# Optimization experiments

Hardware: AMD Instinct MI355X
Metric: run time of the kernel (lower is better)

## Reference

```python
import jax, jax.numpy as jnp
import numpy as np

THRESHOLD = 0.5
NEG_POS_RATIO = 3
ALPHA = 1.0
BETA = 1.0
IGNORE_INDEX = 255

B, P, C, O = 16, 16384, 21, 16
H = W = 256


def cxcy_to_xy(c):
    return jnp.concatenate([c[..., :2] - c[..., 2:] / 2, c[..., :2] + c[..., 2:] / 2], axis=-1)


def xy_to_cxcy(xy):
    return jnp.concatenate([(xy[..., :2] + xy[..., 2:]) / 2, xy[..., 2:] - xy[..., :2]], axis=-1)


def cxcy_to_gcxgcy(cxcy, priors_cxcy):
    return jnp.concatenate([
        (cxcy[..., :2] - priors_cxcy[..., :2]) / (priors_cxcy[..., 2:] / 10.0),
        jnp.log(cxcy[..., 2:] / priors_cxcy[..., 2:]) * 5.0,
    ], axis=-1)


def jaccard(set1, set2):
    # set1 [O,4] xy, set2 [P,4] xy -> IoU [O,P]
    lo = jnp.maximum(set1[:, None, :2], set2[None, :, :2])
    hi = jnp.minimum(set1[:, None, 2:], set2[None, :, 2:])
    wh = jnp.clip(hi - lo, 0.0)
    inter = wh[..., 0] * wh[..., 1]
    a1 = (set1[:, 2] - set1[:, 0]) * (set1[:, 3] - set1[:, 1])
    a2 = (set2[:, 2] - set2[:, 0]) * (set2[:, 3] - set2[:, 1])
    return inter / (a1[:, None] + a2[None, :] - inter)


def setup_inputs() -> dict:
    key = jax.random.key(0)
    ks = jax.random.split(key, 8)
    predicted_locs = jax.random.normal(ks[0], (B, P, 4), dtype=jnp.float32)
    predicted_scores = jax.random.normal(ks[1], (B, P, C), dtype=jnp.float32)
    predicted_masks = jax.random.normal(ks[2], (B, C, H, W), dtype=jnp.float32)
    x1y1 = jax.random.uniform(ks[3], (B, O, 2), dtype=jnp.float32) * 0.8
    wh = jax.random.uniform(ks[4], (B, O, 2), dtype=jnp.float32) * 0.19 + 0.01
    boxes = jnp.concatenate([x1y1, x1y1 + wh], axis=-1)  # valid xy boxes
    pc = jax.random.uniform(ks[5], (P, 2), dtype=jnp.float32) * 0.9 + 0.05
    pwh = jax.random.uniform(ks[6], (P, 2), dtype=jnp.float32) * 0.28 + 0.02
    priors_cxcy = jnp.concatenate([pc, pwh], axis=-1)
    labels = jax.random.randint(ks[7], (B, O), 1, C)  # object labels, never background
    masks = jax.random.randint(jax.random.fold_in(key, 99), (B, 1, H, W), 0, C)
    return {
        'predicted_locs': predicted_locs,
        'predicted_scores': predicted_scores,
        'predicted_masks': predicted_masks,
        'boxes': boxes,
        'priors_cxcy': priors_cxcy,
        'labels': labels,
        'masks': masks,
    }


def _assign(bx, lb, priors_cxcy, priors_xy):
    # bx [O,4] xy, lb [O] int -> true_locs [P,4], true_classes [P]
    ov = jaccard(bx, priors_xy)  # [O,P]
    overlap_for_each_prior = ov.max(axis=0)       # [P]
    object_for_each_prior = ov.argmax(axis=0)     # [P]
    prior_for_each_object = ov.argmax(axis=1)     # [O]
    # guarantee every object is matched to its best prior
    object_for_each_prior = object_for_each_prior.at[prior_for_each_object].set(jnp.arange(O))
    overlap_for_each_prior = overlap_for_each_prior.at[prior_for_each_object].set(1.0)
    label_for_each_prior = lb[object_for_each_prior]
    label_for_each_prior = jnp.where(overlap_for_each_prior < THRESHOLD, 0, label_for_each_prior)
    true_locs = cxcy_to_gcxgcy(xy_to_cxcy(bx[object_for_each_prior]), priors_cxcy)
    return true_locs, label_for_each_prior


def reference(predicted_locs, predicted_scores, predicted_masks, boxes, priors_cxcy, labels, masks):
    priors_xy = cxcy_to_xy(priors_cxcy)
    true_locs, true_classes = jax.vmap(_assign, in_axes=(0, 0, None, None))(
        boxes, labels, priors_cxcy, priors_xy)  # [B,P,4], [B,P]

    pos = true_classes != 0                      # [B,P]
    pos_f = pos.astype(predicted_locs.dtype)
    n_pos = pos.sum(axis=1)                      # [B]

    # localization: L1Loss (mean over positive prior elements)
    diff = jnp.abs(predicted_locs - true_locs)
    loc_loss = (diff * pos_f[..., None]).sum() / jnp.maximum(pos_f.sum() * 4.0, 1.0)

    # confidence: CE per prior + hard negative mining
    logp = jax.nn.log_softmax(predicted_scores, axis=-1)            # [B,P,C]
    ce = -jnp.take_along_axis(logp, true_classes[..., None], axis=-1)[..., 0]  # [B,P]
    ce_pos_sum = (ce * pos_f).sum()
    ce_neg = jnp.where(pos, 0.0, ce)
    ce_neg_sorted = -jnp.sort(-ce_neg, axis=1)                      # descending
    ranks = jnp.arange(P)[None, :]
    hard = (ranks < (NEG_POS_RATIO * n_pos)[:, None]).astype(ce.dtype)
    ce_hardneg_sum = (ce_neg_sorted * hard).sum()
    conf_loss = (ce_hardneg_sum + ce_pos_sum) / n_pos.sum().astype(ce.dtype)

    # mask loss: cross_entropy2d, sum reduction then / (H*W) / B
    tgt = masks[:, 0]                                                # [B,H,W]
    valid = (tgt != IGNORE_INDEX)
    t = jnp.where(valid, tgt, 0)
    logp_m = jax.nn.log_softmax(predicted_masks, axis=1)             # [B,C,H,W]
    ce_m = -jnp.take_along_axis(logp_m, t[:, None], axis=1)[:, 0]    # [B,H,W]
    mask_loss = (ce_m * valid.astype(ce_m.dtype)).sum() / (H * W) / B

    return conf_loss + ALPHA * loc_loss + BETA * mask_loss
```

## Files before the change

kernel.cpp:

```cpp
#include <hip/hip_runtime.h>
#include <cstdint>
#include <cstddef>

#define Bn 16
#define Pn 16384
#define Cn 21
#define On 16
#define HWn 65536
#define THRESH 0.5f


__device__ __forceinline__ float waveReduceSum(float v) {
  for (int off = 32; off > 0; off >>= 1) v += __shfl_down(v, off, 64);
  return v;
}
__device__ __forceinline__ int waveReduceSumI(int v) {
  for (int off = 32; off > 0; off >>= 1) v += __shfl_down(v, off, 64);
  return v;
}

__global__ __launch_bounds__(256) void k_phase1(
    const float* __restrict__ boxes, const float* __restrict__ priors,
    unsigned long long* __restrict__ partials, int* __restrict__ done_cnt) {
  const int lane = threadIdx.x & 63, wave = threadIdx.x >> 6;
  __shared__ float4 sbox[On];
  __shared__ float sarea[On];
  __shared__ unsigned long long skey[On];
  if (blockIdx.x == 0 && threadIdx.x == 0) *done_cnt = 0;

  const int b = blockIdx.x >> 6;
  const int p0 = (blockIdx.x & 63) << 8;
  const int p = p0 + threadIdx.x;
  if (threadIdx.x < On) {
    float4 bx = ((const float4*)boxes)[b * On + threadIdx.x];
    sbox[threadIdx.x] = bx;
    sarea[threadIdx.x] = (bx.z - bx.x) * (bx.w - bx.y);
    skey[threadIdx.x] = 0ULL;
  }
  __syncthreads();
  float4 pr = ((const float4*)priors)[p];
  const float px1 = pr.x - 0.5f * pr.z, py1 = pr.y - 0.5f * pr.w;
  const float px2 = pr.x + 0.5f * pr.z, py2 = pr.y + 0.5f * pr.w;
  const float parea = pr.z * pr.w;
#pragma unroll
  for (int o = 0; o < On; ++o) {
    float4 bx = sbox[o];
    float ix = fmaxf(fminf(px2, bx.z) - fmaxf(px1, bx.x), 0.f);
    float iy = fmaxf(fminf(py2, bx.w) - fmaxf(py1, bx.y), 0.f);
    float inter = ix * iy;
    float iou = inter / (sarea[o] + parea - inter);
    float m = iou;
#pragma unroll
    for (int off = 32; off > 0; off >>= 1) m = fmaxf(m, __shfl_xor(m, off, 64));
    unsigned long long tie = __ballot(iou == m);
    if (lane == 0) {
      int lmin = __ffsll(tie) - 1;
      unsigned minp = (unsigned)(p0 + (wave << 6) + lmin);
      unsigned long long key = ((unsigned long long)__float_as_uint(m) << 32) |
                               (unsigned long long)(0xFFFFFFFFu - minp);
      atomicMax(&skey[o], key);
    }
  }
  __syncthreads();
  if (threadIdx.x < On)
    partials[(size_t)blockIdx.x * On + threadIdx.x] = skey[threadIdx.x];
}

__global__ __launch_bounds__(256, 2) void k_assign(
    const float* __restrict__ plocs, const float* __restrict__ pscores,
    const float* __restrict__ boxes, const float* __restrict__ priors,
    const int* __restrict__ labels, const unsigned long long* __restrict__ partials,
    float* __restrict__ ce_neg, float* __restrict__ apart_loc,
    float* __restrict__ apart_ce, int* __restrict__ apart_npos) {
  __shared__ float ssc[256 * Cn];
  __shared__ float4 sbox[On];
  __shared__ float sarea[On];
  __shared__ int slab[On];
  __shared__ int spfo[On];
  __shared__ unsigned long long skey[On];
  __shared__ float sr1[4], sr2[4];
  __shared__ int sri[4];
  const int lane = threadIdx.x & 63, wave = threadIdx.x >> 6;
  const int b = blockIdx.x >> 6;
  const int p0 = (blockIdx.x & 63) << 8;
  const int p = p0 + threadIdx.x;
  {
    const float4* src = (const float4*)(pscores + ((size_t)b * Pn + p0) * Cn);
    float4* dst = (float4*)ssc;
#pragma unroll
    for (int i = threadIdx.x; i < (256 * Cn) / 4; i += 256) dst[i] = src[i];
  }
  if (threadIdx.x < On) {
    float4 bx = ((const float4*)boxes)[b * On + threadIdx.x];
    sbox[threadIdx.x] = bx;
    sarea[threadIdx.x] = (bx.z - bx.x) * (bx.w - bx.y);
    slab[threadIdx.x] = labels[b * On + threadIdx.x];
    skey[threadIdx.x] = 0ULL;
  }
  __syncthreads();
  {
    const int o = threadIdx.x & 15, j = threadIdx.x >> 4;
    const unsigned long long* pp = partials + ((size_t)b * 64) * On;
    unsigned long long k = 0ULL;
#pragma unroll
    for (int t = 0; t < 4; ++t) {
      unsigned long long v = pp[(size_t)(j * 4 + t) * On + o];
      k = v > k ? v : k;
    }
    atomicMax(&skey[o], k);
  }
  __syncthreads();
  if (threadIdx.x < On)
    spfo[threadIdx.x] = (int)(0xFFFFFFFFu - (unsigned)(skey[threadIdx.x] & 0xFFFFFFFFULL));
  __syncthreads();

  float4 pr = ((const float4*)priors)[p];
  const float px1 = pr.x - 0.5f * pr.z, py1 = pr.y - 0.5f * pr.w;
  const float px2 = pr.x + 0.5f * pr.z, py2 = pr.y + 0.5f * pr.w;
  const float parea = pr.z * pr.w;
  float best = -1.f;
  int bobj = 0;
#pragma unroll
  for (int o = 0; o < On; ++o) {
    float4 bx = sbox[o];
    float ix = fmaxf(fminf(px2, bx.z) - fmaxf(px1, bx.x), 0.f);
    float iy = fmaxf(fminf(py2, bx.w) - fmaxf(py1, bx.y), 0.f);
    float inter = ix * iy;
    float iou = inter / (sarea[o] + parea - inter);
    if (iou > best) { best = iou; bobj = o; }
  }
#pragma unroll
  for (int o = 0; o < On; ++o) {
    if (spfo[o] == p) { bobj = o; best = 1.0f; }
  }
  const int lbl = (best < THRESH) ? 0 : slab[bobj];
  const bool pos = (lbl != 0);
  float locp = 0.f;
  if (pos) {
    float4 bx = sbox[bobj];
    float cx = 0.5f * (bx.x + bx.z), cy = 0.5f * (bx.y + bx.w);
    float w = bx.z - bx.x, h = bx.w - bx.y;
    float g0 = (cx - pr.x) / (pr.z * 0.1f);
    float g1 = (cy - pr.y) / (pr.w * 0.1f);
    float g2 = logf(w / pr.z) * 5.f;
    float g3 = logf(h / pr.w) * 5.f;
    float4 pl = ((const float4*)plocs)[b * Pn + p];
    locp = fabsf(pl.x - g0) + fabsf(pl.y - g1) + fabsf(pl.z - g2) + fabsf(pl.w - g3);
  }
  const float* my = ssc + threadIdx.x * Cn;
  float s = 0.f, xt = 0.f;
#pragma unroll
  for (int c = 0; c < Cn; ++c) {
    float v = my[c];
    s += __expf(v);
    if (c == lbl) xt = v;
  }
  float ce = __logf(s) - xt;
  ce_neg[b * Pn + p] = pos ? 0.f : ce;
  float cep = pos ? ce : 0.f;

  float r1 = waveReduceSum(locp);
  float r2 = waveReduceSum(cep);
  int ri = waveReduceSumI(pos ? 1 : 0);
  if (lane == 0) { sr1[wave] = r1; sr2[wave] = r2; sri[wave] = ri; }
  __syncthreads();
  if (threadIdx.x == 0) {
    apart_loc[blockIdx.x] = sr1[0] + sr1[1] + sr1[2] + sr1[3];
    apart_ce[blockIdx.x] = sr2[0] + sr2[1] + sr2[2] + sr2[3];
    apart_npos[blockIdx.x] = sri[0] + sri[1] + sri[2] + sri[3];
  }
}

__global__ __launch_bounds__(1024) void k_hnmask_final(
    const float* __restrict__ ce_neg, const int* __restrict__ apart_npos,
    const float* __restrict__ apart_loc, const float* __restrict__ apart_ce,
    const float* __restrict__ pm, const int* __restrict__ msk,
    float* __restrict__ bres, float* __restrict__ mpart,
    int* __restrict__ done_cnt, float* __restrict__ out) {
  const int tid = threadIdx.x;
  const int lane = tid & 63, wave = tid >> 6;
  __shared__ int scnt[16];
  __shared__ float ssum[16];
  __shared__ float sce[16], smk[16], shn[16];
  __shared__ int sK;
  __shared__ int stick;

  if (blockIdx.x < Bn) {
    const int b = blockIdx.x;
    unsigned rv[16];
#pragma unroll
    for (int i = 0; i < 16; ++i)
      rv[i] = __float_as_uint(ce_neg[b * Pn + i * 1024 + tid]);
    if (wave == 0) {
      int v = apart_npos[b * 64 + lane];
      v = waveReduceSumI(v);
      if (lane == 0) sK = v;
    }
    __syncthreads();
    int K = 3 * sK;
    if (K > Pn) K = Pn;
    unsigned lo = 0u, hi = 0x7F800000u;
    while (lo < hi) {
      unsigned mid = lo + ((hi - lo) >> 1);
      int c = 0;
#pragma unroll
      for (int i = 0; i < 16; ++i) c += (rv[i] > mid) ? 1 : 0;
      c = waveReduceSumI(c);
      if (lane == 0) scnt[wave] = c;
      __syncthreads();
      int total = 0;
#pragma unroll
      for (int w = 0; w < 16; ++w) total += scnt[w];
      if (total < K) hi = mid; else lo = mid + 1;
      __syncthreads();
    }
    const float fv = __uint_as_float(lo);
    float s = 0.f;
    int c = 0;
#pragma unroll
    for (int i = 0; i < 16; ++i) {
      if (rv[i] > lo) { s += __uint_as_float(rv[i]); c++; }
    }
    s = waveReduceSum(s);
    c = waveReduceSumI(c);
    if (lane == 0) { ssum[wave] = s; scnt[wave] = c; }
    __syncthreads();
    if (tid == 0) {
      float tots = 0.f;
      int totc = 0;
#pragma unroll
      for (int w = 0; w < 16; ++w) { tots += ssum[w]; totc += scnt[w]; }
      bres[b] = tots + (float)(K - totc) * fv;
    }
  } else {
    const int t = blockIdx.x - Bn;
    const int idx4 = t * 1024 + tid;
    const int b = idx4 >> 14;
    const int pix = (idx4 & 16383) << 2;
    int4 t4 = ((const int4*)msk)[idx4];
    const float* base = pm + (size_t)b * ((size_t)Cn * HWn) + pix;
#define M_LD(i) (*(const float4*)(base + (size_t)(i) * HWn))
    float4 q0 = M_LD(0), q1 = M_LD(1), q2 = M_LD(2), q3 = M_LD(3);
    float4 q4 = M_LD(4), q5 = M_LD(5), q6 = M_LD(6), q7 = M_LD(7);
    const bool w0 = (t4.x != 255), w1 = (t4.y != 255), w2 = (t4.z != 255),
               w3 = (t4.w != 255);
    const int c0 = w0 ? t4.x : 0, c1 = w1 ? t4.y : 0, c2 = w2 ? t4.z : 0,
              c3 = w3 ? t4.w : 0;
    float s0 = 0.f, s1 = 0.f, s2 = 0.f, s3 = 0.f;
    float x0 = 0.f, x1 = 0.f, x2 = 0.f, x3 = 0.f;
#define M_ACC(v, c)                                                         \
  {                                                                         \
    s0 += __expf(v.x); s1 += __expf(v.y);                                   \
    s2 += __expf(v.z); s3 += __expf(v.w);                                   \
    if (c0 == c) x0 = v.x; if (c1 == c) x1 = v.y;                           \
    if (c2 == c) x2 = v.z; if (c3 == c) x3 = v.w;                           \
  }
#define M_STEP(r, c, pf) { float4 tt = r; r = M_LD(pf); M_ACC(tt, c) }
    M_STEP(q0, 0, 8)  M_STEP(q1, 1, 9)  M_STEP(q2, 2, 10) M_STEP(q3, 3, 11)
    M_STEP(q4, 4, 12) M_STEP(q5, 5, 13) M_STEP(q6, 6, 14) M_STEP(q7, 7, 15)
    M_STEP(q0, 8, 16) M_STEP(q1, 9, 17) M_STEP(q2, 10, 18) M_STEP(q3, 11, 19)
    M_STEP(q4, 12, 20)
    M_ACC(q5, 13) M_ACC(q6, 14) M_ACC(q7, 15) M_ACC(q0, 16)
    M_ACC(q1, 17) M_ACC(q2, 18) M_ACC(q3, 19) M_ACC(q4, 20)
#undef M_STEP
#undef M_ACC
#undef M_LD
    float contrib = (w0 ? (__logf(s0) - x0) : 0.f) +
                    (w1 ? (__logf(s1) - x1) : 0.f) +
                    (w2 ? (__logf(s2) - x2) : 0.f) +
                    (w3 ? (__logf(s3) - x3) : 0.f);
    float r = waveReduceSum(contrib);
    if (lane == 0) ssum[wave] = r;
    __syncthreads();
    if (tid == 0) {
      float acc = 0.f;
#pragma unroll
      for (int w = 0; w < 16; ++w) acc += ssum[w];
      mpart[t] = acc;
    }
  }

  __syncthreads();
  if (tid == 0) {
    __threadfence();
    stick = atomicAdd(done_cnt, 1);
  }
  __syncthreads();
  if (stick != Bn + 256 - 1) return;
  __threadfence();
  float l_loc = apart_loc[tid];
  float l_ce = apart_ce[tid];
  int l_np = apart_npos[tid];
  float l_msk = (tid < 256) ? atomicAdd(&mpart[tid], 0.f) : 0.f;
  float l_hn = (tid < Bn) ? atomicAdd(&bres[tid], 0.f) : 0.f;
  l_loc = waveReduceSum(l_loc);
  l_ce = waveReduceSum(l_ce);
  l_msk = waveReduceSum(l_msk);
  l_hn = waveReduceSum(l_hn);
  int l_npw = waveReduceSumI(l_np);
  if (lane == 0) {
    ssum[wave] = l_loc;
    sce[wave] = l_ce;
    smk[wave] = l_msk;
    shn[wave] = l_hn;
    scnt[wave] = l_npw;
  }
  __syncthreads();
  if (tid == 0) {
    float a0 = 0.f, a1 = 0.f, a2 = 0.f, a3 = 0.f;
    int np_i = 0;
#pragma unroll
    for (int w = 0; w < 16; ++w) {
      a0 += ssum[w]; a1 += sce[w]; a3 += smk[w]; a2 += shn[w];
      np_i += scnt[w];
    }
    float np = (float)np_i;
    float conf = (a2 + a1) / np;
    float loc = a0 / fmaxf(np * 4.f, 1.f);
    float maskl = a3 / (float)HWn / (float)Bn;
    out[0] = conf + loc + maskl;
  }
}

extern "C" void kernel_launch(void* const* d_in, const int* in_sizes, int n_in,
                              void* d_out, int out_size, void* d_ws, size_t ws_size,
                              hipStream_t stream) {
  const float* plocs   = (const float*)d_in[0];
  const float* pscores = (const float*)d_in[1];
  const float* pmasks  = (const float*)d_in[2];
  const float* boxes   = (const float*)d_in[3];
  const float* priors  = (const float*)d_in[4];
  const int*   labels  = (const int*)d_in[5];
  const int*   masks   = (const int*)d_in[6];

  char* ws = (char*)d_ws;
  float* mpart = (float*)ws;
  unsigned long long* partials = (unsigned long long*)(ws + 4096);
  float* ce_neg = (float*)(ws + 135168);
  float* apart_loc = (float*)(ws + 1183744);
  float* apart_ce = (float*)(ws + 1187840);
  int* apart_npos = (int*)(ws + 1191936);
  float* bres = (float*)(ws + 1196032);
  int* done_cnt = (int*)(ws + 1196160);

  k_phase1<<<1024, 256, 0, stream>>>(boxes, priors, partials, done_cnt);
  k_assign<<<1024, 256, 0, stream>>>(plocs, pscores, boxes, priors, labels,
                                     partials, ce_neg, apart_loc, apart_ce,
                                     apart_npos);
  k_hnmask_final<<<Bn + 256, 1024, 0, stream>>>(ce_neg, apart_npos, apart_loc,
                                                apart_ce, pmasks, masks, bres,
                                                mpart, done_cnt, (float*)d_out);
}
```

Baseline: 195.7 us.

## Halve block size and issue all 21 mask-channel loads upfront via inline asm

```diff
diff --git a/kernel.cpp b/kernel.cpp
--- a/kernel.cpp
+++ b/kernel.cpp
@@ -8,6 +8,8 @@
 #define On 16
 #define HWn 65536
 #define THRESH 0.5f
+
+typedef float f4v __attribute__((ext_vector_type(4)));
 
 
 __device__ __forceinline__ float waveReduceSum(float v) {
@@ -171,7 +173,7 @@
   }
 }
 
-__global__ __launch_bounds__(1024) void k_hnmask_final(
+__global__ __launch_bounds__(512, 4) void k_hnmask_final(
     const float* __restrict__ ce_neg, const int* __restrict__ apart_npos,
     const float* __restrict__ apart_loc, const float* __restrict__ apart_ce,
     const float* __restrict__ pm, const int* __restrict__ msk,
@@ -179,18 +181,18 @@
     int* __restrict__ done_cnt, float* __restrict__ out) {
   const int tid = threadIdx.x;
   const int lane = tid & 63, wave = tid >> 6;
-  __shared__ int scnt[16];
-  __shared__ float ssum[16];
-  __shared__ float sce[16], smk[16], shn[16];
+  __shared__ int scnt[8];
+  __shared__ float ssum[8];
+  __shared__ float sce[8], smk[8], shn[8];
   __shared__ int sK;
   __shared__ int stick;
 
   if (blockIdx.x < Bn) {
     const int b = blockIdx.x;
-    unsigned rv[16];
-#pragma unroll
-    for (int i = 0; i < 16; ++i)
-      rv[i] = __float_as_uint(ce_neg[b * Pn + i * 1024 + tid]);
+    unsigned rv[32];
+#pragma unroll
+    for (int i = 0; i < 32; ++i)
+      rv[i] = __float_as_uint(ce_neg[b * Pn + i * 512 + tid]);
     if (wave == 0) {
       int v = apart_npos[b * 64 + lane];
       v = waveReduceSumI(v);
@@ -204,13 +206,13 @@
       unsigned mid = lo + ((hi - lo) >> 1);
       int c = 0;
 #pragma unroll
-      for (int i = 0; i < 16; ++i) c += (rv[i] > mid) ? 1 : 0;
+      for (int i = 0; i < 32; ++i) c += (rv[i] > mid) ? 1 : 0;
       c = waveReduceSumI(c);
       if (lane == 0) scnt[wave] = c;
       __syncthreads();
       int total = 0;
 #pragma unroll
-      for (int w = 0; w < 16; ++w) total += scnt[w];
+      for (int w = 0; w < 8; ++w) total += scnt[w];
       if (total < K) hi = mid; else lo = mid + 1;
       __syncthreads();
     }
@@ -218,7 +220,7 @@
     float s = 0.f;
     int c = 0;
 #pragma unroll
-    for (int i = 0; i < 16; ++i) {
+    for (int i = 0; i < 32; ++i) {
       if (rv[i] > lo) { s += __uint_as_float(rv[i]); c++; }
     }
     s = waveReduceSum(s);
@@ -229,53 +231,61 @@
       float tots = 0.f;
       int totc = 0;
 #pragma unroll
-      for (int w = 0; w < 16; ++w) { tots += ssum[w]; totc += scnt[w]; }
+      for (int w = 0; w < 8; ++w) { tots += ssum[w]; totc += scnt[w]; }
       bres[b] = tots + (float)(K - totc) * fv;
     }
   } else {
     const int t = blockIdx.x - Bn;
-    const int idx4 = t * 1024 + tid;
-    const int b = idx4 >> 14;
-    const int pix = (idx4 & 16383) << 2;
-    int4 t4 = ((const int4*)msk)[idx4];
-    const float* base = pm + (size_t)b * ((size_t)Cn * HWn) + pix;
-#define M_LD(i) (*(const float4*)(base + (size_t)(i) * HWn))
-    float4 q0 = M_LD(0), q1 = M_LD(1), q2 = M_LD(2), q3 = M_LD(3);
-    float4 q4 = M_LD(4), q5 = M_LD(5), q6 = M_LD(6), q7 = M_LD(7);
-    const bool w0 = (t4.x != 255), w1 = (t4.y != 255), w2 = (t4.z != 255),
-               w3 = (t4.w != 255);
-    const int c0 = w0 ? t4.x : 0, c1 = w1 ? t4.y : 0, c2 = w2 ? t4.z : 0,
-              c3 = w3 ? t4.w : 0;
-    float s0 = 0.f, s1 = 0.f, s2 = 0.f, s3 = 0.f;
-    float x0 = 0.f, x1 = 0.f, x2 = 0.f, x3 = 0.f;
-#define M_ACC(v, c)                                                         \
-  {                                                                         \
-    s0 += __expf(v.x); s1 += __expf(v.y);                                   \
-    s2 += __expf(v.z); s3 += __expf(v.w);                                   \
-    if (c0 == c) x0 = v.x; if (c1 == c) x1 = v.y;                           \
-    if (c2 == c) x2 = v.z; if (c3 == c) x3 = v.w;                           \
-  }
-#define M_STEP(r, c, pf) { float4 tt = r; r = M_LD(pf); M_ACC(tt, c) }
-    M_STEP(q0, 0, 8)  M_STEP(q1, 1, 9)  M_STEP(q2, 2, 10) M_STEP(q3, 3, 11)
-    M_STEP(q4, 4, 12) M_STEP(q5, 5, 13) M_STEP(q6, 6, 14) M_STEP(q7, 7, 15)
-    M_STEP(q0, 8, 16) M_STEP(q1, 9, 17) M_STEP(q2, 10, 18) M_STEP(q3, 11, 19)
-    M_STEP(q4, 12, 20)
-    M_ACC(q5, 13) M_ACC(q6, 14) M_ACC(q7, 15) M_ACC(q0, 16)
-    M_ACC(q1, 17) M_ACC(q2, 18) M_ACC(q3, 19) M_ACC(q4, 20)
-#undef M_STEP
+    float contrib = 0.f;
+#pragma unroll
+    for (int q = 0; q < 2; ++q) {
+      const int idx4 = t * 1024 + q * 512 + tid;
+      const int b = idx4 >> 14;
+      const int pix = (idx4 & 16383) << 2;
+      int4 t4 = ((const int4*)msk)[idx4];
+      const float* base = pm + (size_t)b * ((size_t)Cn * HWn) + pix;
+#define M_LD(i)                                                              \
+  f4v v##i;                                                                  \
+  {                                                                          \
+    const float* a##i = base + (size_t)(i) * HWn;                            \
+    asm volatile("global_load_dwordx4 %0, %1, off"                           \
+                 : "=&v"(v##i) : "v"(a##i));                                 \
+  }
+      M_LD(0) M_LD(1) M_LD(2) M_LD(3) M_LD(4) M_LD(5) M_LD(6) M_LD(7)
+      M_LD(8) M_LD(9) M_LD(10) M_LD(11) M_LD(12) M_LD(13) M_LD(14) M_LD(15)
+      M_LD(16) M_LD(17) M_LD(18) M_LD(19) M_LD(20)
+#undef M_LD
+      asm volatile("s_waitcnt vmcnt(0)" ::: "memory");
+      __builtin_amdgcn_sched_barrier(0);
+      const bool w0 = (t4.x != 255), w1 = (t4.y != 255), w2 = (t4.z != 255),
+                 w3 = (t4.w != 255);
+      const int c0 = w0 ? t4.x : 0, c1 = w1 ? t4.y : 0, c2 = w2 ? t4.z : 0,
+                c3 = w3 ? t4.w : 0;
+      float s0 = 0.f, s1 = 0.f, s2 = 0.f, s3 = 0.f;
+      float x0 = 0.f, x1 = 0.f, x2 = 0.f, x3 = 0.f;
+#define M_ACC(i)                                                             \
+  {                                                                          \
+    s0 += __expf(v##i.x); s1 += __expf(v##i.y);                              \
+    s2 += __expf(v##i.z); s3 += __expf(v##i.w);                              \
+    if (c0 == i) x0 = v##i.x; if (c1 == i) x1 = v##i.y;                      \
+    if (c2 == i) x2 = v##i.z; if (c3 == i) x3 = v##i.w;                      \
+  }
+      M_ACC(0) M_ACC(1) M_ACC(2) M_ACC(3) M_ACC(4) M_ACC(5) M_ACC(6) M_ACC(7)
+      M_ACC(8) M_ACC(9) M_ACC(10) M_ACC(11) M_ACC(12) M_ACC(13) M_ACC(14)
+      M_ACC(15) M_ACC(16) M_ACC(17) M_ACC(18) M_ACC(19) M_ACC(20)
 #undef M_ACC
-#undef M_LD
-    float contrib = (w0 ? (__logf(s0) - x0) : 0.f) +
-                    (w1 ? (__logf(s1) - x1) : 0.f) +
-                    (w2 ? (__logf(s2) - x2) : 0.f) +
-                    (w3 ? (__logf(s3) - x3) : 0.f);
+      contrib += (w0 ? (__logf(s0) - x0) : 0.f) +
+                 (w1 ? (__logf(s1) - x1) : 0.f) +
+                 (w2 ? (__logf(s2) - x2) : 0.f) +
+                 (w3 ? (__logf(s3) - x3) : 0.f);
+    }
     float r = waveReduceSum(contrib);
     if (lane == 0) ssum[wave] = r;
     __syncthreads();
     if (tid == 0) {
       float acc = 0.f;
 #pragma unroll
-      for (int w = 0; w < 16; ++w) acc += ssum[w];
+      for (int w = 0; w < 8; ++w) acc += ssum[w];
       mpart[t] = acc;
     }
   }
@@ -288,9 +298,9 @@
   __syncthreads();
   if (stick != Bn + 256 - 1) return;
   __threadfence();
-  float l_loc = apart_loc[tid];
-  float l_ce = apart_ce[tid];
-  int l_np = apart_npos[tid];
+  float l_loc = apart_loc[tid] + apart_loc[tid + 512];
+  float l_ce = apart_ce[tid] + apart_ce[tid + 512];
+  int l_np = apart_npos[tid] + apart_npos[tid + 512];
   float l_msk = (tid < 256) ? atomicAdd(&mpart[tid], 0.f) : 0.f;
   float l_hn = (tid < Bn) ? atomicAdd(&bres[tid], 0.f) : 0.f;
   l_loc = waveReduceSum(l_loc);
@@ -310,7 +320,7 @@
     float a0 = 0.f, a1 = 0.f, a2 = 0.f, a3 = 0.f;
     int np_i = 0;
 #pragma unroll
-    for (int w = 0; w < 16; ++w) {
+    for (int w = 0; w < 8; ++w) {
       a0 += ssum[w]; a1 += sce[w]; a3 += smk[w]; a2 += shn[w];
       np_i += scnt[w];
     }
@@ -347,7 +357,7 @@
   k_assign<<<1024, 256, 0, stream>>>(plocs, pscores, boxes, priors, labels,
                                      partials, ce_neg, apart_loc, apart_ce,
                                      apart_npos);
-  k_hnmask_final<<<Bn + 256, 1024, 0, stream>>>(ce_neg, apart_npos, apart_loc,
-                                                apart_ce, pmasks, masks, bres,
-                                                mpart, done_cnt, (float*)d_out);
-}
+  k_hnmask_final<<<Bn + 256, 512, 0, stream>>>(ce_neg, apart_npos, apart_loc,
+                                               apart_ce, pmasks, masks, bres,
+                                               mpart, done_cnt, (float*)d_out);
+}
```

Result: faster. 190.2 us (-2.8%).
